# Optimization experiments

Hardware: AMD Instinct MI355X
Metric: run time of the kernel (lower is better)

## Reference

```python
import jax, jax.numpy as jnp
import numpy as np

K = 9          # kernel_size
CENTER = K // 2
EXTEND = 1.0   # extend_scope
B, C_IN, C_OUT, H, W = 2, 64, 64, 256, 256


def group_norm(x, w, b, groups, eps=1e-5):
    Bx, C, Hx, Wx = x.shape
    xg = x.reshape(Bx, groups, C // groups, Hx, Wx)
    m = xg.mean(axis=(2, 3, 4), keepdims=True)
    v = xg.var(axis=(2, 3, 4), keepdims=True)
    xn = ((xg - m) * jax.lax.rsqrt(v + eps)).reshape(Bx, C, Hx, Wx)
    return xn * w[None, :, None, None] + b[None, :, None, None]


def conv2d(x, w, b, stride, padding):
    y = jax.lax.conv_general_dilated(x, w, stride, padding,
                                     dimension_numbers=('NCHW', 'OIHW', 'NCHW'))
    return y + b[None, :, None, None]


def bilinear_sample(feat, iy, ix):
    # feat [B,C,H,W]; iy/ix pixel coords [B,Hg,Wg]; align_corners=True bilinear
    Hf, Wf = feat.shape[2], feat.shape[3]
    y0 = jnp.floor(iy); x0 = jnp.floor(ix)
    wy1 = iy - y0; wx1 = ix - x0
    wy0 = 1.0 - wy1; wx0 = 1.0 - wx1
    y0i = jnp.clip(y0, 0, Hf - 1).astype(jnp.int32)
    y1i = jnp.clip(y0 + 1, 0, Hf - 1).astype(jnp.int32)
    x0i = jnp.clip(x0, 0, Wf - 1).astype(jnp.int32)
    x1i = jnp.clip(x0 + 1, 0, Wf - 1).astype(jnp.int32)
    g = jax.vmap(lambda f, yi, xi: f[:, yi, xi])  # per-batch gather -> [B,C,Hg,Wg]
    return (g(feat, y0i, x0i) * (wy0 * wx0)[:, None]
            + g(feat, y0i, x1i) * (wy0 * wx1)[:, None]
            + g(feat, y1i, x0i) * (wy1 * wx0)[:, None]
            + g(feat, y1i, x1i) * (wy1 * wx1)[:, None])


def outward_cumsum(off):
    # off [B,K,H,W]: center row -> 0, cumulative sums outward from center
    lower = jnp.flip(jnp.cumsum(jnp.flip(off[:, :CENTER], axis=1), axis=1), axis=1)
    upper = jnp.cumsum(off[:, CENTER + 1:], axis=1)
    zero = jnp.zeros_like(off[:, :1])
    return jnp.concatenate([lower, zero, upper], axis=1)


def reference(x, w_off, b_off, gno_w, gno_b, w_dsc, b_dsc, gn_w, gn_b):
    Bx, _, Hx, Wx = x.shape
    # offset branch: conv3x3 -> GroupNorm(K, 2K) -> tanh
    offset = conv2d(x, w_off, b_off, (1, 1), ((1, 1), (1, 1)))
    offset = jnp.tanh(group_norm(offset, gno_w, gno_b, groups=K))
    y_off = offset[:, :K]                      # morph=0 uses the y half
    y_cum = outward_cumsum(y_off)              # [B,K,H,W]
    y_center = jnp.arange(Hx, dtype=x.dtype)[None, None, :, None]
    x_base = (jnp.arange(Wx, dtype=x.dtype)[None, None, None, :]
              + jnp.linspace(-CENTER, CENTER, K, dtype=x.dtype)[None, :, None, None])
    y_new = y_center + EXTEND * y_cum          # [B,K,H,W]
    x_new = jnp.broadcast_to(x_base, y_new.shape)
    # permute(0,2,1,3).reshape -> [B, K*H, W]
    ycoord = y_new.transpose(0, 2, 1, 3).reshape(Bx, Hx * K, Wx)
    xcoord = x_new.transpose(0, 2, 1, 3).reshape(Bx, Hx * K, Wx)
    # clamp to [0,max] then [-1,1] normalize + align_corners unnormalize == clamp
    iy = jnp.clip(ycoord, 0.0, Hx - 1.0)
    ix = jnp.clip(xcoord, 0.0, Wx - 1.0)
    deformed = bilinear_sample(x, iy, ix)      # [B,C,K*H,W]
    out = conv2d(deformed, w_dsc, b_dsc, (K, 1), 'VALID')  # [B,Cout,H,W]
    out = group_norm(out, gn_w, gn_b, groups=C_OUT // 4)
    return jax.nn.relu(out)


def setup_inputs() -> dict:
    key = jax.random.key(0)
    ks = jax.random.split(key, 3)
    return {
        'x': jax.random.normal(ks[0], (B, C_IN, H, W), dtype=jnp.float32),
        'w_off': jax.random.normal(ks[1], (2 * K, C_IN, 3, 3), dtype=jnp.float32) * 0.05,
        'b_off': jnp.zeros((2 * K,), dtype=jnp.float32),
        'gno_w': jnp.ones((2 * K,), dtype=jnp.float32),
        'gno_b': jnp.zeros((2 * K,), dtype=jnp.float32),
        'w_dsc': jax.random.normal(ks[2], (C_OUT, C_IN, K, 1), dtype=jnp.float32) * 0.05,
        'b_dsc': jnp.zeros((C_OUT,), dtype=jnp.float32),
        'gn_w': jnp.ones((C_OUT,), dtype=jnp.float32),
        'gn_b': jnp.zeros((C_OUT,), dtype=jnp.float32),
    }
```

## Files before the change

kernel.cpp:

```cpp
#include <hip/hip_runtime.h>
#include <hip/hip_fp16.h>
#include <math.h>

#define BB 2
#define CC 64
#define HH 256
#define WW 256
#define KK 9
#define NOFF 10
#define HW (HH*WW)

typedef __attribute__((ext_vector_type(8))) short s16x8;
typedef __attribute__((ext_vector_type(4))) float f32x4;

__device__ __forceinline__ unsigned lerp2h(unsigned a, unsigned b, __half2 fy2) {
    __half2 ah = *(__half2*)&a, bh = *(__half2*)&b;
    __half2 d = __hfma2(fy2, __hsub2(bh, ah), ah);
    return *(unsigned*)&d;
}

__device__ __forceinline__ void swizzle_bhw(int g, int& b, int& h, int& wt) {
    int W = ((g & 7) << 8) | (g >> 3);
    b  = W >> 10;
    int rem = W & 1023;
    h  = rem >> 2;
    wt = rem & 3;
}

__global__ __launch_bounds__(256) void transpose_x_kernel(const float* __restrict__ x,
                                                          unsigned short* __restrict__ xTh,
                                                          const float* __restrict__ w_off,
                                                          const float* __restrict__ w_dsc,
                                                          unsigned short* __restrict__ woffB,
                                                          unsigned short* __restrict__ wdscB) {
    if (blockIdx.x >= 2048) {
        int idx = (blockIdx.x - 2048) * 256 + threadIdx.x;
        if (idx < 18 * 64 * 8) {
            int kb = idx >> 9;
            int L  = (idx >> 3) & 63;
            int j  = idx & 7;
            int n = L & 15, quad = L >> 4;
            int kk = kb * 32 + quad * 8 + j;
            int tap = kk >> 6, ci = kk & 63;
            float v = (n < NOFF) ? w_off[(n * 64 + ci) * 9 + tap] : 0.f;
            __half hv = __float2half(v);
            woffB[idx] = *(unsigned short*)&hv;
        }
        if (idx < 4 * 18 * 64 * 8) {
            int nt = idx / 9216;
            int r  = idx - nt * 9216;
            int kb = r >> 9;
            int L  = (r >> 3) & 63;
            int j  = r & 7;
            int n = L & 15, quad = L >> 4;
            int co = nt * 16 + n;
            int kk = kb * 32 + quad * 8 + j;
            int k = kk >> 6, ci = kk & 63;
            __half hv = __float2half(w_dsc[(co * 64 + ci) * 9 + k]);
            wdscB[idx] = *(unsigned short*)&hv;
        }
        return;
    }
    __shared__ float tile[64 * 65];
    int wt = blockIdx.x & 3;
    int h  = (blockIdx.x >> 2) & 255;
    int b  = blockIdx.x >> 10;
    int w0 = wt * 64;
    int t  = threadIdx.x;
    {
        int wl = t & 63, crow = t >> 6;
        for (int it = 0; it < 16; ++it) {
            int c = crow + it * 4;
            tile[wl * 65 + c] = x[(((b * CC + c) * HH + h) * WW) + w0 + wl];
        }
    }
    __syncthreads();
    {
        int c2 = t & 31, wrow = t >> 5;
        unsigned* dst = (unsigned*)xTh;
        for (int it = 0; it < 8; ++it) {
            int wl = wrow + it * 8;
            __half2 p = __floats2half2_rn(tile[wl * 65 + c2 * 2], tile[wl * 65 + c2 * 2 + 1]);
            dst[(((b * HH + h) * WW) + w0 + wl) * 32 + c2] = *(unsigned*)&p;
        }
    }
}

#define CPITCH 72
__global__ __launch_bounds__(256, 4) void conv_off_mfma(const unsigned short* __restrict__ xTh,
                                                        const unsigned short* __restrict__ woffB,
                                                        const float* __restrict__ b_off,
                                                        unsigned short* __restrict__ off_raw,
                                                        float* __restrict__ partials_off) {
    __shared__ unsigned short sx[3 * 66 * CPITCH];
    __shared__ float rs[4][16], rs2[4][16];
    int t = threadIdx.x;
    int L = t & 63, v = t >> 6;
    int b, h, wt;
    swizzle_bhw(blockIdx.x, b, h, wt);
    int w0 = wt << 6;
    int col = L & 15, quad = L >> 4;

#pragma unroll
    for (int it = 0; it < 7; ++it) {
        int linear = it * 256 + t;
        if (linear < 1584) {
            int dy  = linear / 528;
            int rem = linear - dy * 528;
            int px  = rem >> 3, cg = rem & 7;
            int y  = h - 1 + dy;
            int xc = w0 - 1 + px;
            uint4 d = make_uint4(0, 0, 0, 0);
            if ((unsigned)y < 256u && (unsigned)xc < 256u)
                d = *(const uint4*)(xTh + ((size_t)(((b << 8) + y) << 8) + xc) * 64 + cg * 8);
            *(uint4*)&sx[(dy * 66 + px) * CPITCH + cg * 8] = d;
        }
    }

    s16x8 breg[18];
#pragma unroll
    for (int kb = 0; kb < 18; ++kb)
        breg[kb] = *(const s16x8*)(woffB + (kb * 64 + L) * 8);
    __syncthreads();

    f32x4 acc = {0.f, 0.f, 0.f, 0.f};
#pragma unroll
    for (int kb = 0; kb < 18; ++kb) {
        int tap = kb >> 1;
        int dy = tap / 3, dxl = tap % 3;
        int pxl = v * 16 + col + dxl;
        int ci0 = ((kb & 1) << 5) + quad * 8;
        s16x8 a = *(const s16x8*)&sx[(dy * 66 + pxl) * CPITCH + ci0];
        acc = __builtin_amdgcn_mfma_f32_16x16x32_f16(a, breg[kb], acc, 0, 0, 0);
    }
    int oc = col;
    float bo = b_off[oc];
    float s = 0.f, s2 = 0.f;
#pragma unroll
    for (int r = 0; r < 4; ++r) {
        float val = acc[r] + bo;
        if (oc < NOFF) {
            int w = w0 + v * 16 + quad * 4 + r;
            __half hv = __float2half(val);
            off_raw[((b * NOFF + oc) << 16) + (h << 8) + w] = *(unsigned short*)&hv;
        }
        s += val; s2 += val * val;
    }
    s  += __shfl_xor(s, 16, 64);  s  += __shfl_xor(s, 32, 64);
    s2 += __shfl_xor(s2, 16, 64); s2 += __shfl_xor(s2, 32, 64);
    if (quad == 0) { rs[v][oc] = s; rs2[v][oc] = s2; }
    __syncthreads();
    if (t < NOFF) {
        float a_ = rs[0][t] + rs[1][t] + rs[2][t] + rs[3][t];
        float a2 = rs2[0][t] + rs2[1][t] + rs2[2][t] + rs2[3][t];
        partials_off[(size_t)blockIdx.x * 20 + t * 2]     = a_;
        partials_off[(size_t)blockIdx.x * 20 + t * 2 + 1] = a2;
    }
}

__global__ __launch_bounds__(256) void reduce_off_kernel(const float* __restrict__ partials,
                                                         float* __restrict__ stats) {
    int bg = blockIdx.x;
    int t = threadIdx.x;
    float s = 0.f, s2 = 0.f;
    int b = bg / 5, gg = bg - b * 5;
    for (int i = t; i < 2048; i += 256) {
        int blk_b = (((i & 7) << 8) | (i >> 3)) >> 10;
        if (blk_b == b) {
            const float* p = partials + (size_t)i * 20 + gg * 4;
            s  += p[0] + p[2];
            s2 += p[1] + p[3];
        }
    }
    __shared__ float rs[256], rs2[256];
    rs[t] = s; rs2[t] = s2;
    __syncthreads();
    for (int o = 128; o > 0; o >>= 1) {
        if (t < o) { rs[t] += rs[t + o]; rs2[t] += rs2[t + o]; }
        __syncthreads();
    }
    if (t == 0) {
        float mean = rs[0] * (1.f / 131072.f);
        float var  = rs2[0] * (1.f / 131072.f) - mean * mean;
        stats[bg * 2]     = mean;
        stats[bg * 2 + 1] = rsqrtf(var + 1e-5f);
    }
}

__global__ __launch_bounds__(256) void reduce_out_kernel(const float* __restrict__ partials,
                                                         float* __restrict__ stats) {
    int bg = blockIdx.x;
    int b = bg >> 4, g = bg & 15;
    int t = threadIdx.x;
    float s = 0.f, s2 = 0.f;
    for (int i = t; i < 2048; i += 256) {
        int blk_b = (((i & 7) << 8) | (i >> 3)) >> 10;
        if (blk_b == b) {
            const float* p = partials + (size_t)i * 32 + g * 2;
            s  += p[0];
            s2 += p[1];
        }
    }
    __shared__ float rs[256], rs2[256];
    rs[t] = s; rs2[t] = s2;
    __syncthreads();
    for (int o = 128; o > 0; o >>= 1) {
        if (t < o) { rs[t] += rs[t + o]; rs2[t] += rs2[t + o]; }
        __syncthreads();
    }
    if (t == 0) {
        float mean = rs[0] * (1.f / 262144.f);
        float var  = rs2[0] * (1.f / 262144.f) - mean * mean;
        stats[bg * 2]     = mean;
        stats[bg * 2 + 1] = rsqrtf(var + 1e-5f);
    }
}

__global__ __launch_bounds__(256, 4) void main_mfma(const unsigned short* __restrict__ xTh,
                                                    const unsigned short* __restrict__ off_raw,
                                                    const float* __restrict__ stats_off,
                                                    const float* __restrict__ gno_w,
                                                    const float* __restrict__ gno_b,
                                                    const unsigned short* __restrict__ wdscB,
                                                    const float* __restrict__ b_dsc,
                                                    unsigned short* __restrict__ tmph,
                                                    float* __restrict__ partials_out) {
    __shared__ unsigned short aT[32 * 584];
    __shared__ unsigned       coordA[576];

    int t = threadIdx.x;
    int L = t & 63, nt = t >> 6;
    int b, h, wt;
    swizzle_bhw(blockIdx.x, b, h, wt);
    int w0 = wt << 6;

    if (t < 64) {
        int w = w0 + t;
        float tk[9];
#pragma unroll
        for (int k = 0; k < 9; ++k) {
            unsigned short u = off_raw[((b * NOFF + k) << 16) + (h << 8) + w];
            float vv = __half2float(*(__half*)&u);
            int g = k >> 1;
            float mean = stats_off[(b * 5 + g) * 2];
            float rstd = stats_off[(b * 5 + g) * 2 + 1];
            tk[k] = tanhf((vv - mean) * rstd * gno_w[k] + gno_b[k]);
        }
        float yc[9];
        float c = 0.f;
#pragma unroll
        for (int k = 3; k >= 0; --k) { c += tk[k]; yc[k] = c; }
        yc[4] = 0.f;
        c = 0.f;
#pragma unroll
        for (int k = 5; k < 9; ++k) { c += tk[k]; yc[k] = c; }
#pragma unroll
        for (int k = 0; k < 9; ++k) {
            float y = fminf(fmaxf((float)h + yc[k], 0.f), 255.f);
            float y0f = floorf(y);
            int y0 = (int)y0f;
            int xc = min(max(w + k - 4, 0), 255);
            __half fh = __float2half(y - y0f);
            coordA[t * 9 + k] = (unsigned)y0 | ((unsigned)xc << 8)
                              | ((unsigned)(*(unsigned short*)&fh) << 16);
        }
    }

    s16x8 wreg[18];
#pragma unroll
    for (int kb = 0; kb < 18; ++kb)
        wreg[kb] = *(const s16x8*)(wdscB + ((nt * 18 + kb) * 64 + L) * 8);

    int col = L & 15, quad = L >> 4;
    int co = nt * 16 + col;
    float bias = b_dsc[co];
    float ss = 0.f, ss2 = 0.f;
    int bBase = b << 22;

    for (int round = 0; round < 2; ++round) {
        __syncthreads();
#pragma unroll
        for (int it = 0; it < 9; ++it) {
            int idx = it * 256 + t;
            int cg  = idx & 7;
            int r2  = idx >> 3;
            int pxl = r2 / 9;
            int k   = r2 - pxl * 9;
            int pi  = (round * 32 + pxl) * 9 + k;
            unsigned pc = coordA[pi];
            int o0 = bBase + ((pc & 255) << 14) + (((pc >> 8) & 255) << 6) + cg * 8;
            unsigned short fb = (unsigned short)(pc >> 16);
            int o1 = fb ? o0 + 16384 : o0;
            __half fh = *(__half*)&fb;
            __half2 fy2 = __half2half2(fh);
            uint4 u0 = *(const uint4*)(xTh + o0);
            uint4 u1 = *(const uint4*)(xTh + o1);
            uint4 d;
            d.x = lerp2h(u0.x, u1.x, fy2);
            d.y = lerp2h(u0.y, u1.y, fy2);
            d.z = lerp2h(u0.z, u1.z, fy2);
            d.w = lerp2h(u0.w, u1.w, fy2);
            int c2 = (cg + k) & 7;
            *(uint4*)&aT[pxl * 584 + k * 64 + c2 * 8] = d;
        }
        __syncthreads();

#pragma unroll
        for (int sub = 0; sub < 2; ++sub) {
            int row = sub * 16 + col;
            f32x4 acc = {0.f, 0.f, 0.f, 0.f};
#pragma unroll
            for (int kb = 0; kb < 18; ++kb) {
                int k  = kb >> 1;
                int cch = ((kb & 1) << 2) + quad;
                int c2 = (cch + k) & 7;
                s16x8 a = *(const s16x8*)&aT[row * 584 + k * 64 + c2 * 8];
                acc = __builtin_amdgcn_mfma_f32_16x16x32_f16(a, wreg[kb], acc, 0, 0, 0);
            }
            int wbase = w0 + round * 32 + sub * 16 + quad * 4;
            size_t obase = ((size_t)((b << 16) + (h << 8) + wbase)) * 64 + co;
#pragma unroll
            for (int r = 0; r < 4; ++r) {
                float val = acc[r] + bias;
                ss += val; ss2 += val * val;
                __half hv = __float2half(val);
                tmph[obase + (size_t)r * 64] = *(unsigned short*)&hv;
            }
        }
    }
    ss  += __shfl_xor(ss, 16, 64);  ss  += __shfl_xor(ss, 32, 64);
    ss2 += __shfl_xor(ss2, 16, 64); ss2 += __shfl_xor(ss2, 32, 64);
    float sg = ss, sg2 = ss2;
    sg  += __shfl_xor(sg, 1, 64);  sg  += __shfl_xor(sg, 2, 64);
    sg2 += __shfl_xor(sg2, 1, 64); sg2 += __shfl_xor(sg2, 2, 64);
    if (quad == 0 && (col & 3) == 0) {
        int gi = nt * 4 + (col >> 2);
        partials_out[(size_t)blockIdx.x * 32 + gi * 2]     = sg;
        partials_out[(size_t)blockIdx.x * 32 + gi * 2 + 1] = sg2;
    }
}

__global__ __launch_bounds__(256) void apply_final_kernel(const unsigned short* __restrict__ tmph,
                                                          const float* __restrict__ stats_out,
                                                          const float* __restrict__ gn_w,
                                                          const float* __restrict__ gn_b,
                                                          float* __restrict__ out) {
    __shared__ float tile[64 * 65];
    int wt = blockIdx.x & 3;
    int h  = (blockIdx.x >> 2) & 255;
    int b  = blockIdx.x >> 10;
    int w0 = wt * 64;
    int t  = threadIdx.x;
    {
        int c2 = t & 31, wrow = t >> 5;
        int co0 = c2 * 2;
        int g = co0 >> 2;
        float mean = stats_out[(b * 16 + g) * 2];
        float rstd = stats_out[(b * 16 + g) * 2 + 1];
        float sc0 = rstd * gn_w[co0],     sh0 = gn_b[co0]     - mean * sc0;
        float sc1 = rstd * gn_w[co0 + 1], sh1 = gn_b[co0 + 1] - mean * sc1;
        const unsigned* src = (const unsigned*)tmph;
        for (int it = 0; it < 8; ++it) {
            int wl = wrow + it * 8;
            unsigned u = src[(((b * HH + h) * WW) + w0 + wl) * 32 + c2];
            float2 f = __half22float2(*(__half2*)&u);
            tile[co0 * 65 + wl]       = fmaxf(fmaf(f.x, sc0, sh0), 0.f);
            tile[(co0 + 1) * 65 + wl] = fmaxf(fmaf(f.y, sc1, sh1), 0.f);
        }
    }
    __syncthreads();
    {
        int wl = t & 63, crow = t >> 6;
        for (int it = 0; it < 16; ++it) {
            int co = crow + it * 4;
            out[((size_t)(b * CC + co) * HH + h) * WW + w0 + wl] = tile[co * 65 + wl];
        }
    }
}

extern "C" void kernel_launch(void* const* d_in, const int* in_sizes, int n_in,
                              void* d_out, int out_size, void* d_ws, size_t ws_size,
                              hipStream_t stream) {
    const float* x     = (const float*)d_in[0];
    const float* w_off = (const float*)d_in[1];
    const float* b_off = (const float*)d_in[2];
    const float* gno_w = (const float*)d_in[3];
    const float* gno_b = (const float*)d_in[4];
    const float* w_dsc = (const float*)d_in[5];
    const float* b_dsc = (const float*)d_in[6];
    const float* gn_w  = (const float*)d_in[7];
    const float* gn_b  = (const float*)d_in[8];
    float* out = (float*)d_out;

    char* ws = (char*)d_ws;
    unsigned short* xTh     = (unsigned short*)(ws);
    unsigned short* tmph    = (unsigned short*)(ws + 16777216);
    unsigned short* off_raw = (unsigned short*)(ws + 33554432);
    unsigned short* wdscB   = (unsigned short*)(ws + 36175872);
    unsigned short* woffB   = (unsigned short*)(ws + 36249600);
    float* stats_off        = (float*)(ws + 36268032);
    float* stats_out        = (float*)(ws + 36268288);
    float* partials_off     = (float*)(ws + 36268544);
    float* partials_out     = (float*)(ws + 36432384);

    hipLaunchKernelGGL(transpose_x_kernel, dim3(2192), dim3(256), 0, stream,
                       x, xTh, w_off, w_dsc, woffB, wdscB);
    hipLaunchKernelGGL(conv_off_mfma, dim3(2048), dim3(256), 0, stream,
                       xTh, woffB, b_off, off_raw, partials_off);
    hipLaunchKernelGGL(reduce_off_kernel, dim3(10), dim3(256), 0, stream,
                       partials_off, stats_off);
    hipLaunchKernelGGL(main_mfma, dim3(2048), dim3(256), 0, stream,
                       xTh, off_raw, stats_off, gno_w, gno_b, wdscB, b_dsc,
                       tmph, partials_out);
    hipLaunchKernelGGL(reduce_out_kernel, dim3(32), dim3(256), 0, stream,
                       partials_out, stats_out);
    hipLaunchKernelGGL(apply_final_kernel, dim3(2048), dim3(256), 0, stream,
                       tmph, stats_out, gn_w, gn_b, out);
}
```

Baseline: 160.2 us.

## Vectorize transpose and final-apply memory ops, add MFMA priority and fast tanh

```diff
diff --git a/kernel.cpp b/kernel.cpp
--- a/kernel.cpp
+++ b/kernel.cpp
@@ -17,6 +17,11 @@
     __half2 ah = *(__half2*)&a, bh = *(__half2*)&b;
     __half2 d = __hfma2(fy2, __hsub2(bh, ah), ah);
     return *(unsigned*)&d;
+}
+
+__device__ __forceinline__ float fast_tanh(float z) {
+    float e = __builtin_amdgcn_exp2f(z * 2.885390081777927f);
+    return 1.f - 2.f * __builtin_amdgcn_rcpf(e + 1.f);
 }
 
 __device__ __forceinline__ void swizzle_bhw(int g, int& b, int& h, int& wt) {
@@ -68,20 +73,33 @@
     int w0 = wt * 64;
     int t  = threadIdx.x;
     {
-        int wl = t & 63, crow = t >> 6;
-        for (int it = 0; it < 16; ++it) {
-            int c = crow + it * 4;
-            tile[wl * 65 + c] = x[(((b * CC + c) * HH + h) * WW) + w0 + wl];
+        int wq = t & 15, c0 = t >> 4;
+#pragma unroll
+        for (int it = 0; it < 4; ++it) {
+            int c = c0 + it * 16;
+            float4 v = *(const float4*)&x[(((b * CC + c) * HH + h) * WW) + w0 + wq * 4];
+            tile[(wq * 4 + 0) * 65 + c] = v.x;
+            tile[(wq * 4 + 1) * 65 + c] = v.y;
+            tile[(wq * 4 + 2) * 65 + c] = v.z;
+            tile[(wq * 4 + 3) * 65 + c] = v.w;
         }
     }
     __syncthreads();
     {
-        int c2 = t & 31, wrow = t >> 5;
-        unsigned* dst = (unsigned*)xTh;
-        for (int it = 0; it < 8; ++it) {
-            int wl = wrow + it * 8;
-            __half2 p = __floats2half2_rn(tile[wl * 65 + c2 * 2], tile[wl * 65 + c2 * 2 + 1]);
-            dst[(((b * HH + h) * WW) + w0 + wl) * 32 + c2] = *(unsigned*)&p;
+        int c8 = t & 7, wr = t >> 3;
+        uint4* dst = (uint4*)xTh;
+#pragma unroll
+        for (int it = 0; it < 2; ++it) {
+            int wl = wr + it * 32;
+            const float* row = &tile[wl * 65 + c8 * 8];
+            __half2 p0 = __floats2half2_rn(row[0], row[1]);
+            __half2 p1 = __floats2half2_rn(row[2], row[3]);
+            __half2 p2 = __floats2half2_rn(row[4], row[5]);
+            __half2 p3 = __floats2half2_rn(row[6], row[7]);
+            uint4 d;
+            d.x = *(unsigned*)&p0; d.y = *(unsigned*)&p1;
+            d.z = *(unsigned*)&p2; d.w = *(unsigned*)&p3;
+            dst[((size_t)((b * HH + h) * WW) + w0 + wl) * 8 + c8] = d;
         }
     }
 }
@@ -124,6 +142,7 @@
     __syncthreads();
 
     f32x4 acc = {0.f, 0.f, 0.f, 0.f};
+    __builtin_amdgcn_s_setprio(1);
 #pragma unroll
     for (int kb = 0; kb < 18; ++kb) {
         int tap = kb >> 1;
@@ -133,6 +152,7 @@
         s16x8 a = *(const s16x8*)&sx[(dy * 66 + pxl) * CPITCH + ci0];
         acc = __builtin_amdgcn_mfma_f32_16x16x32_f16(a, breg[kb], acc, 0, 0, 0);
     }
+    __builtin_amdgcn_s_setprio(0);
     int oc = col;
     float bo = b_off[oc];
     float s = 0.f, s2 = 0.f;
@@ -244,7 +264,7 @@
             int g = k >> 1;
             float mean = stats_off[(b * 5 + g) * 2];
             float rstd = stats_off[(b * 5 + g) * 2 + 1];
-            tk[k] = tanhf((vv - mean) * rstd * gno_w[k] + gno_b[k]);
+            tk[k] = fast_tanh((vv - mean) * rstd * gno_w[k] + gno_b[k]);
         }
         float yc[9];
         float c = 0.f;
@@ -309,6 +329,7 @@
         for (int sub = 0; sub < 2; ++sub) {
             int row = sub * 16 + col;
             f32x4 acc = {0.f, 0.f, 0.f, 0.f};
+            __builtin_amdgcn_s_setprio(1);
 #pragma unroll
             for (int kb = 0; kb < 18; ++kb) {
                 int k  = kb >> 1;
@@ -317,6 +338,7 @@
                 s16x8 a = *(const s16x8*)&aT[row * 584 + k * 64 + c2 * 8];
                 acc = __builtin_amdgcn_mfma_f32_16x16x32_f16(a, wreg[kb], acc, 0, 0, 0);
             }
+            __builtin_amdgcn_s_setprio(0);
             int wbase = w0 + round * 32 + sub * 16 + quad * 4;
             size_t obase = ((size_t)((b << 16) + (h << 8) + wbase)) * 64 + co;
 #pragma unroll
@@ -352,28 +374,46 @@
     int w0 = wt * 64;
     int t  = threadIdx.x;
     {
-        int c2 = t & 31, wrow = t >> 5;
-        int co0 = c2 * 2;
-        int g = co0 >> 2;
-        float mean = stats_out[(b * 16 + g) * 2];
-        float rstd = stats_out[(b * 16 + g) * 2 + 1];
-        float sc0 = rstd * gn_w[co0],     sh0 = gn_b[co0]     - mean * sc0;
-        float sc1 = rstd * gn_w[co0 + 1], sh1 = gn_b[co0 + 1] - mean * sc1;
-        const unsigned* src = (const unsigned*)tmph;
-        for (int it = 0; it < 8; ++it) {
-            int wl = wrow + it * 8;
-            unsigned u = src[(((b * HH + h) * WW) + w0 + wl) * 32 + c2];
-            float2 f = __half22float2(*(__half2*)&u);
-            tile[co0 * 65 + wl]       = fmaxf(fmaf(f.x, sc0, sh0), 0.f);
-            tile[(co0 + 1) * 65 + wl] = fmaxf(fmaf(f.y, sc1, sh1), 0.f);
+        int c8 = t & 7, wr = t >> 3;
+        int co0 = c8 * 8;
+        float sc[8], sh[8];
+#pragma unroll
+        for (int j = 0; j < 8; ++j) {
+            int g = (co0 + j) >> 2;
+            float mean = stats_out[(b * 16 + g) * 2];
+            float rstd = stats_out[(b * 16 + g) * 2 + 1];
+            sc[j] = rstd * gn_w[co0 + j];
+            sh[j] = gn_b[co0 + j] - mean * sc[j];
+        }
+        const uint4* src = (const uint4*)tmph;
+#pragma unroll
+        for (int it = 0; it < 2; ++it) {
+            int wl = wr + it * 32;
+            uint4 u = src[((size_t)((b * HH + h) * WW) + w0 + wl) * 8 + c8];
+            float2 f0 = __half22float2(*(__half2*)&u.x);
+            float2 f1 = __half22float2(*(__half2*)&u.y);
+            float2 f2 = __half22float2(*(__half2*)&u.z);
+            float2 f3 = __half22float2(*(__half2*)&u.w);
+            tile[(co0 + 0) * 65 + wl] = fmaxf(fmaf(f0.x, sc[0], sh[0]), 0.f);
+            tile[(co0 + 1) * 65 + wl] = fmaxf(fmaf(f0.y, sc[1], sh[1]), 0.f);
+            tile[(co0 + 2) * 65 + wl] = fmaxf(fmaf(f1.x, sc[2], sh[2]), 0.f);
+            tile[(co0 + 3) * 65 + wl] = fmaxf(fmaf(f1.y, sc[3], sh[3]), 0.f);
+            tile[(co0 + 4) * 65 + wl] = fmaxf(fmaf(f2.x, sc[4], sh[4]), 0.f);
+            tile[(co0 + 5) * 65 + wl] = fmaxf(fmaf(f2.y, sc[5], sh[5]), 0.f);
+            tile[(co0 + 6) * 65 + wl] = fmaxf(fmaf(f3.x, sc[6], sh[6]), 0.f);
+            tile[(co0 + 7) * 65 + wl] = fmaxf(fmaf(f3.y, sc[7], sh[7]), 0.f);
         }
     }
     __syncthreads();
     {
-        int wl = t & 63, crow = t >> 6;
-        for (int it = 0; it < 16; ++it) {
-            int co = crow + it * 4;
-            out[((size_t)(b * CC + co) * HH + h) * WW + w0 + wl] = tile[co * 65 + wl];
+        int wq = t & 15, c0 = t >> 4;
+#pragma unroll
+        for (int it = 0; it < 4; ++it) {
+            int co = c0 + it * 16;
+            const float* row = &tile[co * 65 + wq * 4];
+            float4 v;
+            v.x = row[0]; v.y = row[1]; v.z = row[2]; v.w = row[3];
+            *(float4*)&out[((size_t)(b * CC + co) * HH + h) * WW + w0 + wq * 4] = v;
         }
     }
 }
```

New measurement: 157.9 us. Within noise of the previous version (-1.4%).
